# Kernel optimization log

Measured on AMD Instinct MI355X. Metric: run time of the kernel, lower is better.

The kernel has to match this reference:

```python
import jax, jax.numpy as jnp
import numpy as np

NEG_SLOPE = 0.2  # LeakyReLU slope used by standard GAT


def setup_inputs() -> dict:
    key = jax.random.key(0)
    k1, k2, k3, k4, k5, k6 = jax.random.split(key, 6)
    N, E, F_in, F_out = 100000, 1600000, 256, 128
    x = jax.random.normal(k1, (N, F_in), dtype=jnp.float32)
    edge_index = jax.random.randint(k2, (2, E), 0, N, dtype=jnp.int32)
    W = jax.random.normal(k3, (F_in, F_out), dtype=jnp.float32) * (1.0 / np.sqrt(F_in))
    a_src = jax.random.normal(k4, (F_out,), dtype=jnp.float32) * 0.1
    a_dst = jax.random.normal(k5, (F_out,), dtype=jnp.float32) * 0.1
    return {"x": x, "edge_index": edge_index, "W": W, "a_src": a_src, "a_dst": a_dst}


def reference(x, edge_index, W, a_src, a_dst):
    N = x.shape[0]
    src, dst = edge_index[0], edge_index[1]

    Wh = x @ W                               # [N, F_out]
    alpha_src = Wh @ a_src                   # [N]
    alpha_dst = Wh @ a_dst                   # [N]

    e = alpha_src[src] + alpha_dst[dst]      # [E] raw edge scores
    e = jnp.where(e > 0, e, NEG_SLOPE * e)   # LeakyReLU(0.2)

    # segment softmax over incoming edges of each destination node
    seg_max = jax.ops.segment_max(e, dst, num_segments=N)          # [N]
    seg_max = jnp.where(jnp.isfinite(seg_max), seg_max, 0.0)
    e_exp = jnp.exp(e - seg_max[dst])                               # [E]
    denom = jax.ops.segment_sum(e_exp, dst, num_segments=N)         # [N]
    alpha = e_exp / (denom[dst] + 1e-16)                            # [E]

    # weighted aggregation of source messages
    msgs = alpha[:, None] * Wh[src]                                  # [E, F_out]
    out = jax.ops.segment_sum(msgs, dst, num_segments=N)             # [N, F_out]
    return jax.nn.elu(out)
```

## Files before the change

kernel.cpp:

```cpp
#include <hip/hip_runtime.h>
#include <math.h>

#define NEG_SLOPE 0.2f
#define BINSH 8
#define BCAP 6144

typedef __attribute__((ext_vector_type(8))) short bf16x8;
typedef __attribute__((ext_vector_type(4))) float f32x4;

__device__ inline unsigned short f2b(float f) {
  union { float f; unsigned u; } v; v.f = f;
  unsigned r = v.u + 0x7fffu + ((v.u >> 16) & 1u);
  return (unsigned short)(r >> 16);
}

__global__ void k_prepW(const float* __restrict__ W, unsigned short* __restrict__ WtB,
                        int* __restrict__ cursor, int NBUK) {
  int t = blockIdx.x * blockDim.x + threadIdx.x;
  int k = t >> 7, n = t & 127;
  WtB[n * 256 + k] = f2b(W[(size_t)k * 128 + n]);
  if (blockIdx.x == 0)
    for (int c = threadIdx.x; c < NBUK; c += 256) cursor[c] = c * BCAP;
}

__launch_bounds__(256, 4)
__global__ void k_gemm(const float* __restrict__ x, const unsigned short* __restrict__ WtB,
                       const float* __restrict__ a_src, const float* __restrict__ a_dst,
                       unsigned short* __restrict__ WhB, float* __restrict__ asrc,
                       float* __restrict__ adst, int N) {
  __shared__ unsigned short Cs[128 * 136];
  int t = threadIdx.x;
  int lane = t & 63, wid = t >> 6;
  int lr = lane & 15, lh = lane >> 4;
  int m0 = blockIdx.x * 128;
  int row0 = m0 + wid * 32 + lr;
  int row1 = row0 + 16;
  int r0c = row0 < N ? row0 : N - 1;
  int r1c = row1 < N ? row1 : N - 1;
  const float* xp0 = x + (size_t)r0c * 256 + lh * 8;
  const float* xp1 = x + (size_t)r1c * 256 + lh * 8;

  f32x4 acc[2][8];
#pragma unroll
  for (int rf = 0; rf < 2; ++rf)
#pragma unroll
    for (int f = 0; f < 8; ++f) acc[rf][f] = (f32x4){0.f, 0.f, 0.f, 0.f};

#pragma unroll
  for (int ks = 0; ks < 8; ++ks) {
    float4 u0 = *(const float4*)(xp0 + ks * 32);
    float4 u1 = *(const float4*)(xp0 + ks * 32 + 4);
    float4 v0 = *(const float4*)(xp1 + ks * 32);
    float4 v1 = *(const float4*)(xp1 + ks * 32 + 4);
    bf16x8 a0, a1;
    a0[0] = (short)f2b(u0.x); a0[1] = (short)f2b(u0.y);
    a0[2] = (short)f2b(u0.z); a0[3] = (short)f2b(u0.w);
    a0[4] = (short)f2b(u1.x); a0[5] = (short)f2b(u1.y);
    a0[6] = (short)f2b(u1.z); a0[7] = (short)f2b(u1.w);
    a1[0] = (short)f2b(v0.x); a1[1] = (short)f2b(v0.y);
    a1[2] = (short)f2b(v0.z); a1[3] = (short)f2b(v0.w);
    a1[4] = (short)f2b(v1.x); a1[5] = (short)f2b(v1.y);
    a1[6] = (short)f2b(v1.z); a1[7] = (short)f2b(v1.w);
#pragma unroll
    for (int f = 0; f < 8; ++f) {
      bf16x8 b = *(const bf16x8*)(WtB + ((lr + 16 * f) * 256 + ks * 32 + lh * 8));
      acc[0][f] = __builtin_amdgcn_mfma_f32_16x16x32_bf16(a0, b, acc[0][f], 0, 0, 0);
      acc[1][f] = __builtin_amdgcn_mfma_f32_16x16x32_bf16(a1, b, acc[1][f], 0, 0, 0);
    }
  }

  float asv[8], adv[8];
#pragma unroll
  for (int f = 0; f < 8; ++f) { asv[f] = a_src[lr + 16 * f]; adv[f] = a_dst[lr + 16 * f]; }
  float as_p[2][4] = {}, ad_p[2][4] = {};
#pragma unroll
  for (int rf = 0; rf < 2; ++rf)
#pragma unroll
    for (int f = 0; f < 8; ++f)
#pragma unroll
      for (int r = 0; r < 4; ++r) {
        as_p[rf][r] += acc[rf][f][r] * asv[f];
        ad_p[rf][r] += acc[rf][f][r] * adv[f];
      }
#pragma unroll
  for (int off = 1; off < 16; off <<= 1)
#pragma unroll
    for (int rf = 0; rf < 2; ++rf)
#pragma unroll
      for (int r = 0; r < 4; ++r) {
        as_p[rf][r] += __shfl_xor(as_p[rf][r], off);
        ad_p[rf][r] += __shfl_xor(ad_p[rf][r], off);
      }
  if (lr == 0) {
#pragma unroll
    for (int rf = 0; rf < 2; ++rf)
#pragma unroll
      for (int r = 0; r < 4; ++r) {
        int m = m0 + wid * 32 + rf * 16 + lh * 4 + r;
        if (m < N) { asrc[m] = as_p[rf][r]; adst[m] = ad_p[rf][r]; }
      }
  }

#pragma unroll
  for (int rf = 0; rf < 2; ++rf)
#pragma unroll
    for (int f = 0; f < 8; ++f)
#pragma unroll
      for (int r = 0; r < 4; ++r)
        Cs[(wid * 32 + rf * 16 + lh * 4 + r) * 136 + lr + 16 * f] = f2b(acc[rf][f][r]);
  __syncthreads();
#pragma unroll
  for (int i = 0; i < 8; ++i) {
    int chunk = i * 256 + t;
    int row = chunk >> 4, c8 = chunk & 15;
    int m = m0 + row;
    if (m < N) {
      bf16x8 v = *(const bf16x8*)(Cs + row * 136 + c8 * 8);
      *(bf16x8*)(WhB + (size_t)m * 128 + c8 * 8) = v;
    }
  }
}

__launch_bounds__(256)
__global__ void k_binA(const int* __restrict__ src, const int* __restrict__ dst,
                       int* __restrict__ cursor, unsigned* __restrict__ binned, int E, int NBUK) {
  __shared__ int lh[512];
  int t = threadIdx.x;
  for (int c = t; c < NBUK; c += 256) lh[c] = 0;
  __syncthreads();
  int base = blockIdx.x * 2048;
  int bq[8], rq[8]; unsigned pq[8];
#pragma unroll
  for (int q = 0; q < 8; ++q) {
    int j = base + q * 256 + t;
    if (j < E) {
      int d = dst[j], s = src[j];
      bq[q] = d >> BINSH;
      pq[q] = ((unsigned)s << 8) | (unsigned)(d & 255);
      rq[q] = atomicAdd(&lh[bq[q]], 1);
    } else bq[q] = -1;
  }
  __syncthreads();
  for (int c = t; c < NBUK; c += 256) { int cnt = lh[c]; if (cnt) lh[c] = atomicAdd(&cursor[c], cnt); }
  __syncthreads();
#pragma unroll
  for (int q = 0; q < 8; ++q)
    if (bq[q] >= 0) binned[lh[bq[q]] + rq[q]] = pq[q];
}

__launch_bounds__(256)
__global__ void k_binB(const unsigned* __restrict__ binned, const int* __restrict__ cursor,
                       int* __restrict__ offsets, int* __restrict__ degs,
                       int* __restrict__ csr, int N) {
  int b = blockIdx.x, t = threadIdx.x;
  int lane = t & 63, wid = t >> 6;
  int beg = b * BCAP, end = cursor[b];
  int node0 = b << BINSH;
  int nn = N - node0; if (nn > 256) nn = 256; if (nn < 0) nn = 0;
  __shared__ int ldeg[256];
  __shared__ int lcur[256];
  __shared__ int wp[4];
  ldeg[t] = 0;
  __syncthreads();
  for (int j = beg + t; j < end; j += 256) atomicAdd(&ldeg[binned[j] & 255u], 1);
  __syncthreads();
  int v = (t < nn) ? ldeg[t] : 0;
  int incl = v;
#pragma unroll
  for (int off = 1; off < 64; off <<= 1) { int u = __shfl_up(incl, off); if (lane >= off) incl += u; }
  if (lane == 63) wp[wid] = incl;
  __syncthreads();
  int add = 0;
  for (int k = 0; k < wid; ++k) add += wp[k];
  int ex = add + incl - v;
  if (t < nn) { offsets[node0 + t] = beg + ex; degs[node0 + t] = v; lcur[t] = ex; }
  __syncthreads();
  for (int j = beg + t; j < end; j += 256) {
    unsigned e = binned[j];
    int r = atomicAdd(&lcur[e & 255u], 1);
    csr[beg + r] = (int)(e >> 8);
  }
}

__launch_bounds__(256)
__global__ void k_agg(const int* __restrict__ csr, const int* __restrict__ offsets,
                      const int* __restrict__ degs,
                      const unsigned short* __restrict__ WhB, const float* __restrict__ asrc,
                      const float* __restrict__ adst, float* __restrict__ out, int N) {
  int gt = blockIdx.x * blockDim.x + threadIdx.x;
  int wave = gt >> 6;
  int lane = gt & 63;
  int lq = lane & 15;
  int g = lane >> 4;
  int node = wave * 4 + g;
  if (node >= N) return;
  int beg = offsets[node];
  int end = beg + degs[node];
  float ad = adst[node];
  float acc[8] = {};
  float psum = 0.f;
  for (int chunk = beg; chunk < end; chunk += 16) {
    int j = chunk + lq;
    float p = 0.f; int mys = 0;
    if (j < end) {
      mys = csr[j];
      float e = asrc[mys] + ad;
      e = e > 0.f ? e : NEG_SLOPE * e;
      p = __expf(e);
    }
    psum += p;
#pragma unroll
    for (int tt = 0; tt < 8; ++tt) {
      float pt = __shfl(p, tt, 16);
      int st = __shfl(mys, tt, 16);
      uint4 v = *(const uint4*)(WhB + (size_t)(unsigned)st * 128u + lq * 8);
      acc[0] = fmaf(pt, __uint_as_float(v.x << 16), acc[0]);
      acc[1] = fmaf(pt, __uint_as_float(v.x & 0xffff0000u), acc[1]);
      acc[2] = fmaf(pt, __uint_as_float(v.y << 16), acc[2]);
      acc[3] = fmaf(pt, __uint_as_float(v.y & 0xffff0000u), acc[3]);
      acc[4] = fmaf(pt, __uint_as_float(v.z << 16), acc[4]);
      acc[5] = fmaf(pt, __uint_as_float(v.z & 0xffff0000u), acc[5]);
      acc[6] = fmaf(pt, __uint_as_float(v.w << 16), acc[6]);
      acc[7] = fmaf(pt, __uint_as_float(v.w & 0xffff0000u), acc[7]);
    }
    __builtin_amdgcn_sched_barrier(0);
#pragma unroll
    for (int tt = 8; tt < 16; ++tt) {
      float pt = __shfl(p, tt, 16);
      int st = __shfl(mys, tt, 16);
      uint4 v = *(const uint4*)(WhB + (size_t)(unsigned)st * 128u + lq * 8);
      acc[0] = fmaf(pt, __uint_as_float(v.x << 16), acc[0]);
      acc[1] = fmaf(pt, __uint_as_float(v.x & 0xffff0000u), acc[1]);
      acc[2] = fmaf(pt, __uint_as_float(v.y << 16), acc[2]);
      acc[3] = fmaf(pt, __uint_as_float(v.y & 0xffff0000u), acc[3]);
      acc[4] = fmaf(pt, __uint_as_float(v.z << 16), acc[4]);
      acc[5] = fmaf(pt, __uint_as_float(v.z & 0xffff0000u), acc[5]);
      acc[6] = fmaf(pt, __uint_as_float(v.w << 16), acc[6]);
      acc[7] = fmaf(pt, __uint_as_float(v.w & 0xffff0000u), acc[7]);
    }
  }
  psum += __shfl_xor(psum, 1);
  psum += __shfl_xor(psum, 2);
  psum += __shfl_xor(psum, 4);
  psum += __shfl_xor(psum, 8);
  float inv = 1.f / (psum + 1e-16f);
  size_t obase = (size_t)node * 128 + lq * 8;
  float r[8];
#pragma unroll
  for (int i = 0; i < 8; ++i) {
    float o = acc[i] * inv;
    r[i] = o > 0.f ? o : __expf(o) - 1.f;
  }
  f32x4 lo = {r[0], r[1], r[2], r[3]};
  f32x4 hi = {r[4], r[5], r[6], r[7]};
  __builtin_nontemporal_store(lo, (f32x4*)(out + obase));
  __builtin_nontemporal_store(hi, (f32x4*)(out + obase + 4));
}

extern "C" void kernel_launch(void* const* d_in, const int* in_sizes, int n_in,
                              void* d_out, int out_size, void* d_ws, size_t ws_size,
                              hipStream_t stream) {
  const float* x = (const float*)d_in[0];
  const int* ei = (const int*)d_in[1];
  const float* W = (const float*)d_in[2];
  const float* a_src = (const float*)d_in[3];
  const float* a_dst = (const float*)d_in[4];
  int N = in_sizes[0] / 256;
  int E = in_sizes[1] / 2;
  const int* src = ei;
  const int* dst = ei + E;
  float* out = (float*)d_out;
  int NBUK = (N + 255) >> BINSH;
  size_t REG = (size_t)NBUK * BCAP;

  unsigned short* WhB = (unsigned short*)d_ws;
  unsigned* binned = (unsigned*)(WhB + (size_t)N * 128);
  int* csr = (int*)(binned + REG);
  float* asrc = (float*)(csr + REG);
  float* adst = asrc + N;
  unsigned short* WtB = (unsigned short*)(adst + N);
  int* cursor = (int*)(WtB + 32768);
  int* offsets = cursor + NBUK;
  int* degs = offsets + N;

  k_prepW<<<128, 256, 0, stream>>>(W, WtB, cursor, NBUK);
  k_gemm<<<(N + 127) / 128, 256, 0, stream>>>(x, WtB, a_src, a_dst, WhB, asrc, adst, N);
  k_binA<<<(E + 2047) / 2048, 256, 0, stream>>>(src, dst, cursor, binned, E, NBUK);
  k_binB<<<NBUK, 256, 0, stream>>>(binned, cursor, offsets, degs, csr, N);
  k_agg<<<(N + 15) / 16, 256, 0, stream>>>(csr, offsets, degs, WhB, asrc, adst, out, N);
}
```

Before: 168.3 us.

## Merge W prep with edge binning and GEMM with CSR build into two launches

Folds the weight transpose and the edge-binning pass into one kernel, and the GEMM and per-bucket CSR build into a second kernel, picking the role from the block index. Independent work now runs concurrently and two launch gaps go away. Cursor setup becomes a memset of per-bucket counts, and bucket base offsets are added at use sites. The GEMM kernel's shared-memory footprint and launch bounds now apply to the CSR blocks too, which may lower occupancy for those blocks.

```diff
diff --git a/kernel.cpp b/kernel.cpp
--- a/kernel.cpp
+++ b/kernel.cpp
@@ -14,121 +14,23 @@
   return (unsigned short)(r >> 16);
 }
 
-__global__ void k_prepW(const float* __restrict__ W, unsigned short* __restrict__ WtB,
-                        int* __restrict__ cursor, int NBUK) {
-  int t = blockIdx.x * blockDim.x + threadIdx.x;
-  int k = t >> 7, n = t & 127;
-  WtB[n * 256 + k] = f2b(W[(size_t)k * 128 + n]);
-  if (blockIdx.x == 0)
-    for (int c = threadIdx.x; c < NBUK; c += 256) cursor[c] = c * BCAP;
-}
-
-__launch_bounds__(256, 4)
-__global__ void k_gemm(const float* __restrict__ x, const unsigned short* __restrict__ WtB,
-                       const float* __restrict__ a_src, const float* __restrict__ a_dst,
-                       unsigned short* __restrict__ WhB, float* __restrict__ asrc,
-                       float* __restrict__ adst, int N) {
-  __shared__ unsigned short Cs[128 * 136];
+__launch_bounds__(256)
+__global__ void k_work1(const float* __restrict__ W, unsigned short* __restrict__ WtB,
+                        const int* __restrict__ src, const int* __restrict__ dst,
+                        int* __restrict__ cursor, unsigned* __restrict__ binned,
+                        int E, int NBUK) {
+  int bid = blockIdx.x;
   int t = threadIdx.x;
-  int lane = t & 63, wid = t >> 6;
-  int lr = lane & 15, lh = lane >> 4;
-  int m0 = blockIdx.x * 128;
-  int row0 = m0 + wid * 32 + lr;
-  int row1 = row0 + 16;
-  int r0c = row0 < N ? row0 : N - 1;
-  int r1c = row1 < N ? row1 : N - 1;
-  const float* xp0 = x + (size_t)r0c * 256 + lh * 8;
-  const float* xp1 = x + (size_t)r1c * 256 + lh * 8;
-
-  f32x4 acc[2][8];
-#pragma unroll
-  for (int rf = 0; rf < 2; ++rf)
-#pragma unroll
-    for (int f = 0; f < 8; ++f) acc[rf][f] = (f32x4){0.f, 0.f, 0.f, 0.f};
-
-#pragma unroll
-  for (int ks = 0; ks < 8; ++ks) {
-    float4 u0 = *(const float4*)(xp0 + ks * 32);
-    float4 u1 = *(const float4*)(xp0 + ks * 32 + 4);
-    float4 v0 = *(const float4*)(xp1 + ks * 32);
-    float4 v1 = *(const float4*)(xp1 + ks * 32 + 4);
-    bf16x8 a0, a1;
-    a0[0] = (short)f2b(u0.x); a0[1] = (short)f2b(u0.y);
-    a0[2] = (short)f2b(u0.z); a0[3] = (short)f2b(u0.w);
-    a0[4] = (short)f2b(u1.x); a0[5] = (short)f2b(u1.y);
-    a0[6] = (short)f2b(u1.z); a0[7] = (short)f2b(u1.w);
-    a1[0] = (short)f2b(v0.x); a1[1] = (short)f2b(v0.y);
-    a1[2] = (short)f2b(v0.z); a1[3] = (short)f2b(v0.w);
-    a1[4] = (short)f2b(v1.x); a1[5] = (short)f2b(v1.y);
-    a1[6] = (short)f2b(v1.z); a1[7] = (short)f2b(v1.w);
-#pragma unroll
-    for (int f = 0; f < 8; ++f) {
-      bf16x8 b = *(const bf16x8*)(WtB + ((lr + 16 * f) * 256 + ks * 32 + lh * 8));
-      acc[0][f] = __builtin_amdgcn_mfma_f32_16x16x32_bf16(a0, b, acc[0][f], 0, 0, 0);
-      acc[1][f] = __builtin_amdgcn_mfma_f32_16x16x32_bf16(a1, b, acc[1][f], 0, 0, 0);
-    }
-  }
-
-  float asv[8], adv[8];
-#pragma unroll
-  for (int f = 0; f < 8; ++f) { asv[f] = a_src[lr + 16 * f]; adv[f] = a_dst[lr + 16 * f]; }
-  float as_p[2][4] = {}, ad_p[2][4] = {};
-#pragma unroll
-  for (int rf = 0; rf < 2; ++rf)
-#pragma unroll
-    for (int f = 0; f < 8; ++f)
-#pragma unroll
-      for (int r = 0; r < 4; ++r) {
-        as_p[rf][r] += acc[rf][f][r] * asv[f];
-        ad_p[rf][r] += acc[rf][f][r] * adv[f];
-      }
-#pragma unroll
-  for (int off = 1; off < 16; off <<= 1)
-#pragma unroll
-    for (int rf = 0; rf < 2; ++rf)
-#pragma unroll
-      for (int r = 0; r < 4; ++r) {
-        as_p[rf][r] += __shfl_xor(as_p[rf][r], off);
-        ad_p[rf][r] += __shfl_xor(ad_p[rf][r], off);
-      }
-  if (lr == 0) {
-#pragma unroll
-    for (int rf = 0; rf < 2; ++rf)
-#pragma unroll
-      for (int r = 0; r < 4; ++r) {
-        int m = m0 + wid * 32 + rf * 16 + lh * 4 + r;
-        if (m < N) { asrc[m] = as_p[rf][r]; adst[m] = ad_p[rf][r]; }
-      }
-  }
-
-#pragma unroll
-  for (int rf = 0; rf < 2; ++rf)
-#pragma unroll
-    for (int f = 0; f < 8; ++f)
-#pragma unroll
-      for (int r = 0; r < 4; ++r)
-        Cs[(wid * 32 + rf * 16 + lh * 4 + r) * 136 + lr + 16 * f] = f2b(acc[rf][f][r]);
-  __syncthreads();
-#pragma unroll
-  for (int i = 0; i < 8; ++i) {
-    int chunk = i * 256 + t;
-    int row = chunk >> 4, c8 = chunk & 15;
-    int m = m0 + row;
-    if (m < N) {
-      bf16x8 v = *(const bf16x8*)(Cs + row * 136 + c8 * 8);
-      *(bf16x8*)(WhB + (size_t)m * 128 + c8 * 8) = v;
-    }
-  }
-}
-
-__launch_bounds__(256)
-__global__ void k_binA(const int* __restrict__ src, const int* __restrict__ dst,
-                       int* __restrict__ cursor, unsigned* __restrict__ binned, int E, int NBUK) {
+  if (bid < 128) {
+    int i = bid * 256 + t;
+    int k = i >> 7, n = i & 127;
+    WtB[n * 256 + k] = f2b(W[(size_t)k * 128 + n]);
+    return;
+  }
   __shared__ int lh[512];
-  int t = threadIdx.x;
   for (int c = t; c < NBUK; c += 256) lh[c] = 0;
   __syncthreads();
-  int base = blockIdx.x * 2048;
+  int base = (bid - 128) * 2048;
   int bq[8], rq[8]; unsigned pq[8];
 #pragma unroll
   for (int q = 0; q < 8; ++q) {
@@ -145,40 +47,141 @@
   __syncthreads();
 #pragma unroll
   for (int q = 0; q < 8; ++q)
-    if (bq[q] >= 0) binned[lh[bq[q]] + rq[q]] = pq[q];
-}
-
-__launch_bounds__(256)
-__global__ void k_binB(const unsigned* __restrict__ binned, const int* __restrict__ cursor,
-                       int* __restrict__ offsets, int* __restrict__ degs,
-                       int* __restrict__ csr, int N) {
-  int b = blockIdx.x, t = threadIdx.x;
-  int lane = t & 63, wid = t >> 6;
-  int beg = b * BCAP, end = cursor[b];
-  int node0 = b << BINSH;
-  int nn = N - node0; if (nn > 256) nn = 256; if (nn < 0) nn = 0;
-  __shared__ int ldeg[256];
-  __shared__ int lcur[256];
-  __shared__ int wp[4];
-  ldeg[t] = 0;
-  __syncthreads();
-  for (int j = beg + t; j < end; j += 256) atomicAdd(&ldeg[binned[j] & 255u], 1);
-  __syncthreads();
-  int v = (t < nn) ? ldeg[t] : 0;
-  int incl = v;
-#pragma unroll
-  for (int off = 1; off < 64; off <<= 1) { int u = __shfl_up(incl, off); if (lane >= off) incl += u; }
-  if (lane == 63) wp[wid] = incl;
-  __syncthreads();
-  int add = 0;
-  for (int k = 0; k < wid; ++k) add += wp[k];
-  int ex = add + incl - v;
-  if (t < nn) { offsets[node0 + t] = beg + ex; degs[node0 + t] = v; lcur[t] = ex; }
-  __syncthreads();
-  for (int j = beg + t; j < end; j += 256) {
-    unsigned e = binned[j];
-    int r = atomicAdd(&lcur[e & 255u], 1);
-    csr[beg + r] = (int)(e >> 8);
+    if (bq[q] >= 0) binned[(size_t)bq[q] * BCAP + lh[bq[q]] + rq[q]] = pq[q];
+}
+
+__launch_bounds__(256, 4)
+__global__ void k_work2(const float* __restrict__ x, const unsigned short* __restrict__ WtB,
+                        const float* __restrict__ a_src, const float* __restrict__ a_dst,
+                        unsigned short* __restrict__ WhB, float* __restrict__ asrc,
+                        float* __restrict__ adst, int N, int nGemm,
+                        const unsigned* __restrict__ binned, const int* __restrict__ cursor,
+                        int* __restrict__ offsets, int* __restrict__ degs,
+                        int* __restrict__ csr) {
+  int t = threadIdx.x;
+  if ((int)blockIdx.x < nGemm) {
+    __shared__ unsigned short Cs[128 * 136];
+    int lane = t & 63, wid = t >> 6;
+    int lr = lane & 15, lh2 = lane >> 4;
+    int m0 = blockIdx.x * 128;
+    int row0 = m0 + wid * 32 + lr;
+    int row1 = row0 + 16;
+    int r0c = row0 < N ? row0 : N - 1;
+    int r1c = row1 < N ? row1 : N - 1;
+    const float* xp0 = x + (size_t)r0c * 256 + lh2 * 8;
+    const float* xp1 = x + (size_t)r1c * 256 + lh2 * 8;
+
+    f32x4 acc[2][8];
+#pragma unroll
+    for (int rf = 0; rf < 2; ++rf)
+#pragma unroll
+      for (int f = 0; f < 8; ++f) acc[rf][f] = (f32x4){0.f, 0.f, 0.f, 0.f};
+
+#pragma unroll
+    for (int ks = 0; ks < 8; ++ks) {
+      float4 u0 = *(const float4*)(xp0 + ks * 32);
+      float4 u1 = *(const float4*)(xp0 + ks * 32 + 4);
+      float4 v0 = *(const float4*)(xp1 + ks * 32);
+      float4 v1 = *(const float4*)(xp1 + ks * 32 + 4);
+      bf16x8 a0, a1;
+      a0[0] = (short)f2b(u0.x); a0[1] = (short)f2b(u0.y);
+      a0[2] = (short)f2b(u0.z); a0[3] = (short)f2b(u0.w);
+      a0[4] = (short)f2b(u1.x); a0[5] = (short)f2b(u1.y);
+      a0[6] = (short)f2b(u1.z); a0[7] = (short)f2b(u1.w);
+      a1[0] = (short)f2b(v0.x); a1[1] = (short)f2b(v0.y);
+      a1[2] = (short)f2b(v0.z); a1[3] = (short)f2b(v0.w);
+      a1[4] = (short)f2b(v1.x); a1[5] = (short)f2b(v1.y);
+      a1[6] = (short)f2b(v1.z); a1[7] = (short)f2b(v1.w);
+#pragma unroll
+      for (int f = 0; f < 8; ++f) {
+        bf16x8 b = *(const bf16x8*)(WtB + ((lr + 16 * f) * 256 + ks * 32 + lh2 * 8));
+        acc[0][f] = __builtin_amdgcn_mfma_f32_16x16x32_bf16(a0, b, acc[0][f], 0, 0, 0);
+        acc[1][f] = __builtin_amdgcn_mfma_f32_16x16x32_bf16(a1, b, acc[1][f], 0, 0, 0);
+      }
+    }
+
+    float asv[8], adv[8];
+#pragma unroll
+    for (int f = 0; f < 8; ++f) { asv[f] = a_src[lr + 16 * f]; adv[f] = a_dst[lr + 16 * f]; }
+    float as_p[2][4] = {}, ad_p[2][4] = {};
+#pragma unroll
+    for (int rf = 0; rf < 2; ++rf)
+#pragma unroll
+      for (int f = 0; f < 8; ++f)
+#pragma unroll
+        for (int r = 0; r < 4; ++r) {
+          as_p[rf][r] += acc[rf][f][r] * asv[f];
+          ad_p[rf][r] += acc[rf][f][r] * adv[f];
+        }
+#pragma unroll
+    for (int off = 1; off < 16; off <<= 1)
+#pragma unroll
+      for (int rf = 0; rf < 2; ++rf)
+#pragma unroll
+        for (int r = 0; r < 4; ++r) {
+          as_p[rf][r] += __shfl_xor(as_p[rf][r], off);
+          ad_p[rf][r] += __shfl_xor(ad_p[rf][r], off);
+        }
+    if (lr == 0) {
+#pragma unroll
+      for (int rf = 0; rf < 2; ++rf)
+#pragma unroll
+        for (int r = 0; r < 4; ++r) {
+          int m = m0 + wid * 32 + rf * 16 + lh2 * 4 + r;
+          if (m < N) { asrc[m] = as_p[rf][r]; adst[m] = ad_p[rf][r]; }
+        }
+    }
+
+#pragma unroll
+    for (int rf = 0; rf < 2; ++rf)
+#pragma unroll
+      for (int f = 0; f < 8; ++f)
+#pragma unroll
+        for (int r = 0; r < 4; ++r)
+          Cs[(wid * 32 + rf * 16 + lh2 * 4 + r) * 136 + lr + 16 * f] = f2b(acc[rf][f][r]);
+    __syncthreads();
+#pragma unroll
+    for (int i = 0; i < 8; ++i) {
+      int chunk = i * 256 + t;
+      int row = chunk >> 4, c8 = chunk & 15;
+      int m = m0 + row;
+      if (m < N) {
+        bf16x8 v = *(const bf16x8*)(Cs + row * 136 + c8 * 8);
+        *(bf16x8*)(WhB + (size_t)m * 128 + c8 * 8) = v;
+      }
+    }
+    return;
+  }
+
+  {
+    int b = blockIdx.x - nGemm;
+    int lane = t & 63, wid = t >> 6;
+    int beg = b * BCAP, end = beg + cursor[b];
+    int node0 = b << BINSH;
+    int nn = N - node0; if (nn > 256) nn = 256; if (nn < 0) nn = 0;
+    __shared__ int ldeg[256];
+    __shared__ int lcur[256];
+    __shared__ int wp[4];
+    ldeg[t] = 0;
+    __syncthreads();
+    for (int j = beg + t; j < end; j += 256) atomicAdd(&ldeg[binned[j] & 255u], 1);
+    __syncthreads();
+    int v = (t < nn) ? ldeg[t] : 0;
+    int incl = v;
+#pragma unroll
+    for (int off = 1; off < 64; off <<= 1) { int u = __shfl_up(incl, off); if (lane >= off) incl += u; }
+    if (lane == 63) wp[wid] = incl;
+    __syncthreads();
+    int add = 0;
+    for (int k = 0; k < wid; ++k) add += wp[k];
+    int ex = add + incl - v;
+    if (t < nn) { offsets[node0 + t] = beg + ex; degs[node0 + t] = v; lcur[t] = ex; }
+    __syncthreads();
+    for (int j = beg + t; j < end; j += 256) {
+      unsigned e = binned[j];
+      int r = atomicAdd(&lcur[e & 255u], 1);
+      csr[beg + r] = (int)(e >> 8);
+    }
   }
 }
 
@@ -283,9 +286,12 @@
   int* offsets = cursor + NBUK;
   int* degs = offsets + N;
 
-  k_prepW<<<128, 256, 0, stream>>>(W, WtB, cursor, NBUK);
-  k_gemm<<<(N + 127) / 128, 256, 0, stream>>>(x, WtB, a_src, a_dst, WhB, asrc, adst, N);
-  k_binA<<<(E + 2047) / 2048, 256, 0, stream>>>(src, dst, cursor, binned, E, NBUK);
-  k_binB<<<NBUK, 256, 0, stream>>>(binned, cursor, offsets, degs, csr, N);
+  int nBinA = (E + 2047) / 2048;
+  int nGemm = (N + 127) / 128;
+
+  hipMemsetAsync(cursor, 0, (size_t)NBUK * sizeof(int), stream);
+  k_work1<<<128 + nBinA, 256, 0, stream>>>(W, WtB, src, dst, cursor, binned, E, NBUK);
+  k_work2<<<nGemm + NBUK, 256, 0, stream>>>(x, WtB, a_src, a_dst, WhB, asrc, adst, N, nGemm,
+                                            binned, cursor, offsets, degs, csr);
   k_agg<<<(N + 15) / 16, 256, 0, stream>>>(csr, offsets, degs, WhB, asrc, adst, out, N);
 }
```

Measured after the change: 157.3 us. 1.07x faster.
